# Performance work log

Measured on AMD Instinct MI355X. Metric: run time of the kernel, lower is better.

The kernel has to match this reference:

```python
import jax, jax.numpy as jnp
import numpy as np

# 8 directional offsets (dy, dx) for the -1 tap of each 3x3 filter, filter index 0..7
OFFSETS = [(-1, -1), (-1, 0), (-1, 1), (0, -1), (0, 1), (1, -1), (1, 0), (1, 1)]
# pairing used by the original prod(dim=-1): [[0,4],[1,5],[2,6],[3,7]]
PAIRS = np.array([[0, 4], [1, 5], [2, 6], [3, 7]])


def box_mean(x, k):
    """Uniform k x k box-filter mean with zero padding (same as F.conv2d with ones/k^2)."""
    kern = jnp.ones((1, 1, k, k), x.dtype) / (k * k)
    return jax.lax.conv_general_dilated(
        x, kern, window_strides=(1, 1), padding=[(k // 2, k // 2)] * 2,
        dimension_numbers=('NCHW', 'OIHW', 'NCHW'))


def pcm_scale(l, d):
    """Dilated directional diffs (center minus shifted-by-d neighbor, zero pad),
    opposite-pair products, then min over the 4 pairs."""
    b, c, h, w = l.shape
    p = jnp.pad(l, ((0, 0), (0, 0), (d, d), (d, d)))
    # shifted[..., i][y, x] = l[y + dy*d, x + dx*d] (zeros outside)
    shifted = jnp.stack(
        [p[:, :, d + dy * d:d + dy * d + h, d + dx * d:d + dx * d + w]
         for dy, dx in OFFSETS], axis=-1)  # (b,c,h,w,8)
    diff = l[..., None] - shifted          # PCM_i = conv2d(l, filter_i, dilation=d)
    temp = diff[..., PAIRS].prod(axis=-1)  # (b,c,h,w,4)
    return temp.min(axis=-1)               # (b,c,h,w)


def mpcm(x):
    outs = [pcm_scale(box_mean(x, k), k) for k in (3, 5, 7, 9)]
    return jnp.stack(outs, axis=-1).max(axis=-1)


def setup_inputs() -> dict:
    key = jax.random.key(0)
    input_tensor = jax.random.uniform(key, (16, 1, 512, 512), dtype=jnp.float32)
    return {"input_tensor": input_tensor}


def reference(input_tensor):
    out = mpcm(input_tensor)
    # per-image threshold: mean + 3 * unbiased std (torch .std default ddof=1)
    mean = out.mean(axis=(1, 2, 3), keepdims=True)
    std = out.std(axis=(1, 2, 3), keepdims=True, ddof=1)
    th = mean + 3.0 * std
    return (out > th).astype(out.dtype)
```

## Files before the change

### kernel.cpp

```cpp
#include <hip/hip_runtime.h>


namespace {

constexpr int H = 512, W = 512, NIMG = 16;
constexpr int T = 32;
constexpr int HALO = 13;
constexpr int IN = T + 2 * HALO;
constexpr int TILES = H / T;
constexpr int NT = 256;
constexpr int WI = 61;
constexpr int LSTR = 52;

struct Smem {
  double I[59 * WI];
  union alignas(16) {
    float  inf[IN * 61];
    double L[50 * LSTR];
    double red[8];
  } u;
};

template <int K>
__device__ __forceinline__ void scale_pass(Smem& s, int y0, int x0, double mp[4]) {
  constexpr int R  = K / 2;
  constexpr int LK = T + 2 * K;
  constexpr int HP = LK / 2;
  constexpr int NP = LK * HP;
  constexpr double inv = 1.0 / (double)(K * K);
  const int tid = threadIdx.x;

  for (int pe = tid; pe < NP; pe += NT) {
    const int yy = pe / HP;
    const int xx = (pe - yy * HP) * 2;
    const int iy  = yy + (HALO - K);
    const int ixm = xx + (HALO - K) - R;
    const double* Ia = s.I + (iy - R) * WI + ixm;
    const double* Ib = s.I + (iy + R + 1) * WI + ixm;
    const double a0 = Ia[0], a1 = Ia[1], aK = Ia[K], aK1 = Ia[K + 1];
    const double b0 = Ib[0], b1 = Ib[1], bK = Ib[K], bK1 = Ib[K + 1];
    const double s0 = (bK  - aK)  - (b0 - a0);
    const double s1 = (bK1 - aK1) - (b1 - a1);
    const int gy = y0 - K + yy, gx = x0 - K + xx;
    const bool in0 = ((unsigned)gy < (unsigned)H) & ((unsigned)gx < (unsigned)W);
    const bool in1 = ((unsigned)gy < (unsigned)H) & ((unsigned)(gx + 1) < (unsigned)W);
    double2 o;
    o.x = in0 ? s0 * inv : 0.0;
    o.y = in1 ? s1 * inv : 0.0;
    *(double2*)&s.u.L[yy * LSTR + xx] = o;
  }
  __syncthreads();

#pragma unroll
  for (int j = 0; j < 2; ++j) {
    const int r  = (tid >> 4) + j * 16;
    const int cc = (tid & 15) * 2;
    const double* up  = &s.u.L[r * LSTR + cc];
    const double* mid = &s.u.L[(r + K) * LSTR + cc];
    const double* dn  = &s.u.L[(r + 2 * K) * LSTR + cc];
    const double u0 = up[0],  u1 = up[1],  uK = up[K],  uK1 = up[K + 1],  u2 = up[2 * K],  u21 = up[2 * K + 1];
    const double m0 = mid[0], m1 = mid[1], mK = mid[K], mK1 = mid[K + 1], m2 = mid[2 * K], m21 = mid[2 * K + 1];
    const double w0 = dn[0],  w1 = dn[1],  wK = dn[K],  wK1 = dn[K + 1],  w2 = dn[2 * K],  w21 = dn[2 * K + 1];
    {
      const double c = mK;
      const double e0 = c - u0, e1 = c - uK, e2 = c - u2, e3 = c - m0;
      const double e4 = c - m2, e5 = c - w0, e6 = c - wK, e7 = c - w2;
      const double m = fmin(fmin(e0 * e4, e1 * e5), fmin(e2 * e6, e3 * e7));
      mp[2 * j] = fmax(mp[2 * j], m);
    }
    {
      const double c = mK1;
      const double e0 = c - u1, e1 = c - uK1, e2 = c - u21, e3 = c - m1;
      const double e4 = c - m21, e5 = c - w1, e6 = c - wK1, e7 = c - w21;
      const double m = fmin(fmin(e0 * e4, e1 * e5), fmin(e2 * e6, e3 * e7));
      mp[2 * j + 1] = fmax(mp[2 * j + 1], m);
    }
  }
  __syncthreads();
}

__device__ __forceinline__ void compute_tile(Smem& s, const float* __restrict__ img,
                                             int y0, int x0, double mp[4]) {
  const int tid = threadIdx.x;
  for (int e = tid; e < IN * IN; e += NT) {
    const int iy = e / IN, ix = e - iy * IN;
    const int gy = y0 - HALO + iy, gx = x0 - HALO + ix;
    float v = 0.0f;
    if ((unsigned)gy < (unsigned)H && (unsigned)gx < (unsigned)W) v = img[gy * W + gx];
    s.u.inf[iy * 61 + ix] = v;
  }
  for (int e = tid; e < WI; e += NT) s.I[e] = 0.0;
  for (int e = tid; e < 59; e += NT) s.I[e * WI] = 0.0;
  __syncthreads();

  if (tid < IN) {
    const float* src = &s.u.inf[tid * 61];
    double* dst = &s.I[(tid + 1) * WI + 1];
#pragma unroll
    for (int x = 0; x < IN; x += 2) {
      const float f0 = src[x], f1 = src[x + 1];
      const double r0 = (x ? dst[x - 1] : 0.0);
      const double v0 = r0 + (double)f0;
      const double v1 = v0 + (double)f1;
      dst[x] = v0; dst[x + 1] = v1;
    }
  }
  __syncthreads();

  if (tid < IN) {
    double* p = &s.I[WI + (tid + 1)];
    double run = 0.0;
#pragma unroll
    for (int y = 0; y < IN; y += 2) {
      const double v0 = p[0], v1 = p[WI];
      const double r0 = run + v0;
      run = r0 + v1;
      p[0] = r0; p[WI] = run;
      p += 2 * WI;
    }
  }
  __syncthreads();

  mp[0] = mp[1] = mp[2] = mp[3] = -1.0e300;
  scale_pass<3>(s, y0, x0, mp);
  scale_pass<5>(s, y0, x0, mp);
  scale_pass<7>(s, y0, x0, mp);
  scale_pass<9>(s, y0, x0, mp);
}

__global__ __launch_bounds__(NT, 3) void k_stats(const float* __restrict__ in,
                                                 double* __restrict__ partials,
                                                 double* __restrict__ wsmp) {
  __shared__ Smem s;
  const int img = blockIdx.z, tyb = blockIdx.y, txb = blockIdx.x;
  const int y0 = tyb * T, x0 = txb * T;
  double mp[4];
  compute_tile(s, in + (size_t)img * H * W, y0, x0, mp);

  const int tid = threadIdx.x;
  if (wsmp != nullptr) {
#pragma unroll
    for (int j = 0; j < 2; ++j) {
      const int r = (tid >> 4) + j * 16, cc = (tid & 15) * 2;
      double2 v; v.x = mp[2 * j]; v.y = mp[2 * j + 1];
      *(double2*)&wsmp[(size_t)img * H * W + (size_t)(y0 + r) * W + (x0 + cc)] = v;
    }
  }

  double s1 = (mp[0] + mp[1]) + (mp[2] + mp[3]);
  double s2 = (mp[0] * mp[0] + mp[1] * mp[1]) + (mp[2] * mp[2] + mp[3] * mp[3]);
#pragma unroll
  for (int off = 32; off; off >>= 1) {
    s1 += __shfl_down(s1, off);
    s2 += __shfl_down(s2, off);
  }
  if ((tid & 63) == 0) { s.u.red[tid >> 6] = s1; s.u.red[4 + (tid >> 6)] = s2; }
  __syncthreads();
  if (tid == 0) {
    const int bl = (img * TILES + tyb) * TILES + txb;
    partials[2 * bl]     = (s.u.red[0] + s.u.red[1]) + (s.u.red[2] + s.u.red[3]);
    partials[2 * bl + 1] = (s.u.red[4] + s.u.red[5]) + (s.u.red[6] + s.u.red[7]);
  }
}

__global__ void k_thresh(const double* __restrict__ partials, double* __restrict__ th) {
  const int img = threadIdx.x;
  if (img < NIMG) {
    double S = 0.0, S2 = 0.0;
    const int nb = TILES * TILES;
    for (int b = 0; b < nb; ++b) {
      S  += partials[2 * (img * nb + b)];
      S2 += partials[2 * (img * nb + b) + 1];
    }
    const double N = (double)(H * W);
    const double mean = S / N;
    double var = (S2 - S * S / N) / (N - 1.0);
    if (var < 0.0) var = 0.0;
    th[img] = mean + 3.0 * sqrt(var);
  }
}

__global__ __launch_bounds__(NT) void k_out_cached(const double* __restrict__ wsmp,
                                                   const double* __restrict__ th,
                                                   float* __restrict__ out) {
  const int n = NIMG * H * W / 2;
  for (int i = blockIdx.x * NT + threadIdx.x; i < n; i += gridDim.x * NT) {
    const double t = th[i >> 17];
    const double2 v = ((const double2*)wsmp)[i];
    float2 o; o.x = (v.x > t) ? 1.0f : 0.0f; o.y = (v.y > t) ? 1.0f : 0.0f;
    ((float2*)out)[i] = o;
  }
}

__global__ __launch_bounds__(NT, 3) void k_out_full(const float* __restrict__ in,
                                                    const double* __restrict__ th,
                                                    float* __restrict__ out) {
  __shared__ Smem s;
  const int img = blockIdx.z, tyb = blockIdx.y, txb = blockIdx.x;
  const int y0 = tyb * T, x0 = txb * T;
  double mp[4];
  compute_tile(s, in + (size_t)img * H * W, y0, x0, mp);
  const double t = th[img];
  const int tid = threadIdx.x;
#pragma unroll
  for (int j = 0; j < 2; ++j) {
    const int r = (tid >> 4) + j * 16, cc = (tid & 15) * 2;
    float2 o;
    o.x = (mp[2 * j]     > t) ? 1.0f : 0.0f;
    o.y = (mp[2 * j + 1] > t) ? 1.0f : 0.0f;
    *(float2*)&out[(size_t)img * H * W + (size_t)(y0 + r) * W + (x0 + cc)] = o;
  }
}

}

extern "C" void kernel_launch(void* const* d_in, const int* in_sizes, int n_in,
                              void* d_out, int out_size, void* d_ws, size_t ws_size,
                              hipStream_t stream) {
  const float* in = (const float*)d_in[0];
  float* out = (float*)d_out;

  double* th = (double*)d_ws;
  double* partials = (double*)((char*)d_ws + 4096);
  double* wsmp = (double*)((char*)d_ws + 131072);
  const bool cache = ws_size >= (size_t)131072 + (size_t)NIMG * H * W * 8;

  dim3 grid(TILES, TILES, NIMG);
  k_stats<<<grid, NT, 0, stream>>>(in, partials, cache ? wsmp : nullptr);
  k_thresh<<<1, 64, 0, stream>>>(partials, th);
  if (cache) {
    k_out_cached<<<2048, NT, 0, stream>>>(wsmp, th, out);
  } else {
    k_out_full<<<grid, NT, 0, stream>>>(in, th, out);
  }
}
```

Measured before the change: 110.8 us.

## Switch to 64x16 rectangular tiles and simplify integral-image construction

Changes the per-block tile from 32x32 to 64 wide by 16 tall, so each warp covers full 64-column rows. The input is loaded straight into the double integral-image buffer, and the row and column prefix scans become simple sequential loops instead of a separate float staging pass. The stencil stage now reads neighbors with paired double2 loads. The wider halo-to-tile ratio vertically raises redundant halo work, and the row scan covers 90 columns serially, both traded for better coalescing and fewer passes.

```diff
diff --git a/kernel.cpp b/kernel.cpp
--- a/kernel.cpp
+++ b/kernel.cpp
@@ -4,41 +4,43 @@
 namespace {
 
 constexpr int H = 512, W = 512, NIMG = 16;
-constexpr int T = 32;
+constexpr int TW = 64, TH = 16;
 constexpr int HALO = 13;
-constexpr int IN = T + 2 * HALO;
-constexpr int TILES = H / T;
+constexpr int IR = TH + 2 * HALO + 1;
+constexpr int IC = TW + 2 * HALO + 1;
+constexpr int WI = IC;
 constexpr int NT = 256;
-constexpr int WI = 61;
-constexpr int LSTR = 52;
+constexpr int LS = 82;
 
 struct Smem {
-  double I[59 * WI];
   union alignas(16) {
-    float  inf[IN * 61];
-    double L[50 * LSTR];
+    double L[34 * LS];
     double red[8];
   } u;
+  double I[IR * WI];
 };
 
 template <int K>
 __device__ __forceinline__ void scale_pass(Smem& s, int y0, int x0, double mp[4]) {
-  constexpr int R  = K / 2;
-  constexpr int LK = T + 2 * K;
-  constexpr int HP = LK / 2;
-  constexpr int NP = LK * HP;
+  constexpr int R   = K / 2;
+  constexpr int LH  = TH + 2 * K;
+  constexpr int LW  = TW + 2 * K;
+  constexpr int HPW = LW / 2;
+  constexpr int NP  = LH * HPW;
   constexpr double inv = 1.0 / (double)(K * K);
   const int tid = threadIdx.x;
 
   for (int pe = tid; pe < NP; pe += NT) {
-    const int yy = pe / HP;
-    const int xx = (pe - yy * HP) * 2;
-    const int iy  = yy + (HALO - K);
-    const int ixm = xx + (HALO - K) - R;
-    const double* Ia = s.I + (iy - R) * WI + ixm;
-    const double* Ib = s.I + (iy + R + 1) * WI + ixm;
-    const double a0 = Ia[0], a1 = Ia[1], aK = Ia[K], aK1 = Ia[K + 1];
-    const double b0 = Ib[0], b1 = Ib[1], bK = Ib[K], bK1 = Ib[K + 1];
+    const int yy = pe / HPW;
+    const int xx = (pe - yy * HPW) * 2;
+    const int li = yy + (HALO - K);
+    const int lj = xx + (HALO - K) - R;
+    const double* Ia = s.I + (li - R) * WI + lj;
+    const double* Ib = Ia + K * WI;
+    const double a0 = Ia[0], aK = Ia[K];
+    const double a1 = Ia[1], aK1 = Ia[K + 1];
+    const double b0 = Ib[0], bK = Ib[K];
+    const double b1 = Ib[1], bK1 = Ib[K + 1];
     const double s0 = (bK  - aK)  - (b0 - a0);
     const double s1 = (bK1 - aK1) - (b1 - a1);
     const int gy = y0 - K + yy, gx = x0 - K + xx;
@@ -47,31 +49,37 @@
     double2 o;
     o.x = in0 ? s0 * inv : 0.0;
     o.y = in1 ? s1 * inv : 0.0;
-    *(double2*)&s.u.L[yy * LSTR + xx] = o;
+    *(double2*)&s.u.L[yy * LS + xx] = o;
   }
   __syncthreads();
 
 #pragma unroll
   for (int j = 0; j < 2; ++j) {
-    const int r  = (tid >> 4) + j * 16;
-    const int cc = (tid & 15) * 2;
-    const double* up  = &s.u.L[r * LSTR + cc];
-    const double* mid = &s.u.L[(r + K) * LSTR + cc];
-    const double* dn  = &s.u.L[(r + 2 * K) * LSTR + cc];
-    const double u0 = up[0],  u1 = up[1],  uK = up[K],  uK1 = up[K + 1],  u2 = up[2 * K],  u21 = up[2 * K + 1];
-    const double m0 = mid[0], m1 = mid[1], mK = mid[K], mK1 = mid[K + 1], m2 = mid[2 * K], m21 = mid[2 * K + 1];
-    const double w0 = dn[0],  w1 = dn[1],  wK = dn[K],  wK1 = dn[K + 1],  w2 = dn[2 * K],  w21 = dn[2 * K + 1];
+    const int r  = (tid >> 5) + 8 * j;
+    const int cc = (tid & 31) * 2;
+    const double* up  = &s.u.L[r * LS + cc];
+    const double* mid = up + K * LS;
+    const double* dn  = up + 2 * K * LS;
+    const double2 u0p = *(const double2*)up;
+    const double  uK = up[K], uK1 = up[K + 1];
+    const double2 u2p = *(const double2*)(up + 2 * K);
+    const double2 m0p = *(const double2*)mid;
+    const double  mK = mid[K], mK1 = mid[K + 1];
+    const double2 m2p = *(const double2*)(mid + 2 * K);
+    const double2 w0p = *(const double2*)dn;
+    const double  wK = dn[K], wK1 = dn[K + 1];
+    const double2 w2p = *(const double2*)(dn + 2 * K);
     {
       const double c = mK;
-      const double e0 = c - u0, e1 = c - uK, e2 = c - u2, e3 = c - m0;
-      const double e4 = c - m2, e5 = c - w0, e6 = c - wK, e7 = c - w2;
+      const double e0 = c - u0p.x, e1 = c - uK, e2 = c - u2p.x, e3 = c - m0p.x;
+      const double e4 = c - m2p.x, e5 = c - w0p.x, e6 = c - wK, e7 = c - w2p.x;
       const double m = fmin(fmin(e0 * e4, e1 * e5), fmin(e2 * e6, e3 * e7));
       mp[2 * j] = fmax(mp[2 * j], m);
     }
     {
       const double c = mK1;
-      const double e0 = c - u1, e1 = c - uK1, e2 = c - u21, e3 = c - m1;
-      const double e4 = c - m21, e5 = c - w1, e6 = c - wK1, e7 = c - w21;
+      const double e0 = c - u0p.y, e1 = c - uK1, e2 = c - u2p.y, e3 = c - m0p.y;
+      const double e4 = c - m2p.y, e5 = c - w0p.y, e6 = c - wK1, e7 = c - w2p.y;
       const double m = fmin(fmin(e0 * e4, e1 * e5), fmin(e2 * e6, e3 * e7));
       mp[2 * j + 1] = fmax(mp[2 * j + 1], m);
     }
@@ -82,42 +90,29 @@
 __device__ __forceinline__ void compute_tile(Smem& s, const float* __restrict__ img,
                                              int y0, int x0, double mp[4]) {
   const int tid = threadIdx.x;
-  for (int e = tid; e < IN * IN; e += NT) {
-    const int iy = e / IN, ix = e - iy * IN;
-    const int gy = y0 - HALO + iy, gx = x0 - HALO + ix;
-    float v = 0.0f;
-    if ((unsigned)gy < (unsigned)H && (unsigned)gx < (unsigned)W) v = img[gy * W + gx];
-    s.u.inf[iy * 61 + ix] = v;
-  }
-  for (int e = tid; e < WI; e += NT) s.I[e] = 0.0;
-  for (int e = tid; e < 59; e += NT) s.I[e * WI] = 0.0;
-  __syncthreads();
-
-  if (tid < IN) {
-    const float* src = &s.u.inf[tid * 61];
-    double* dst = &s.I[(tid + 1) * WI + 1];
-#pragma unroll
-    for (int x = 0; x < IN; x += 2) {
-      const float f0 = src[x], f1 = src[x + 1];
-      const double r0 = (x ? dst[x - 1] : 0.0);
-      const double v0 = r0 + (double)f0;
-      const double v1 = v0 + (double)f1;
-      dst[x] = v0; dst[x + 1] = v1;
-    }
-  }
-  __syncthreads();
-
-  if (tid < IN) {
+  for (int e = tid; e < IR * IC; e += NT) {
+    const int iy = e / IC, ix = e - iy * IC;
+    const int gy = y0 - HALO + iy - 1, gx = x0 - HALO + ix - 1;
+    double v = 0.0;
+    if (iy > 0 && ix > 0 && (unsigned)gy < (unsigned)H && (unsigned)gx < (unsigned)W)
+      v = (double)img[gy * W + gx];
+    s.I[iy * WI + ix] = v;
+  }
+  __syncthreads();
+
+  if (tid < IR - 1) {
+    double* p = &s.I[(tid + 1) * WI + 1];
+    double run = 0.0;
+#pragma unroll
+    for (int x = 0; x < IC - 1; ++x) { run += p[x]; p[x] = run; }
+  }
+  __syncthreads();
+
+  if (tid < IC - 1) {
     double* p = &s.I[WI + (tid + 1)];
     double run = 0.0;
 #pragma unroll
-    for (int y = 0; y < IN; y += 2) {
-      const double v0 = p[0], v1 = p[WI];
-      const double r0 = run + v0;
-      run = r0 + v1;
-      p[0] = r0; p[WI] = run;
-      p += 2 * WI;
-    }
+    for (int y = 0; y < IR - 1; ++y) { run += *p; *p = run; p += WI; }
   }
   __syncthreads();
 
@@ -132,8 +127,8 @@
                                                  double* __restrict__ partials,
                                                  double* __restrict__ wsmp) {
   __shared__ Smem s;
-  const int img = blockIdx.z, tyb = blockIdx.y, txb = blockIdx.x;
-  const int y0 = tyb * T, x0 = txb * T;
+  const int img = blockIdx.z;
+  const int y0 = blockIdx.y * TH, x0 = blockIdx.x * TW;
   double mp[4];
   compute_tile(s, in + (size_t)img * H * W, y0, x0, mp);
 
@@ -141,7 +136,7 @@
   if (wsmp != nullptr) {
 #pragma unroll
     for (int j = 0; j < 2; ++j) {
-      const int r = (tid >> 4) + j * 16, cc = (tid & 15) * 2;
+      const int r = (tid >> 5) + 8 * j, cc = (tid & 31) * 2;
       double2 v; v.x = mp[2 * j]; v.y = mp[2 * j + 1];
       *(double2*)&wsmp[(size_t)img * H * W + (size_t)(y0 + r) * W + (x0 + cc)] = v;
     }
@@ -157,7 +152,7 @@
   if ((tid & 63) == 0) { s.u.red[tid >> 6] = s1; s.u.red[4 + (tid >> 6)] = s2; }
   __syncthreads();
   if (tid == 0) {
-    const int bl = (img * TILES + tyb) * TILES + txb;
+    const int bl = (img * gridDim.y + blockIdx.y) * gridDim.x + blockIdx.x;
     partials[2 * bl]     = (s.u.red[0] + s.u.red[1]) + (s.u.red[2] + s.u.red[3]);
     partials[2 * bl + 1] = (s.u.red[4] + s.u.red[5]) + (s.u.red[6] + s.u.red[7]);
   }
@@ -167,7 +162,7 @@
   const int img = threadIdx.x;
   if (img < NIMG) {
     double S = 0.0, S2 = 0.0;
-    const int nb = TILES * TILES;
+    const int nb = (H / TH) * (W / TW);
     for (int b = 0; b < nb; ++b) {
       S  += partials[2 * (img * nb + b)];
       S2 += partials[2 * (img * nb + b) + 1];
@@ -196,15 +191,15 @@
                                                     const double* __restrict__ th,
                                                     float* __restrict__ out) {
   __shared__ Smem s;
-  const int img = blockIdx.z, tyb = blockIdx.y, txb = blockIdx.x;
-  const int y0 = tyb * T, x0 = txb * T;
+  const int img = blockIdx.z;
+  const int y0 = blockIdx.y * TH, x0 = blockIdx.x * TW;
   double mp[4];
   compute_tile(s, in + (size_t)img * H * W, y0, x0, mp);
   const double t = th[img];
   const int tid = threadIdx.x;
 #pragma unroll
   for (int j = 0; j < 2; ++j) {
-    const int r = (tid >> 4) + j * 16, cc = (tid & 15) * 2;
+    const int r = (tid >> 5) + 8 * j, cc = (tid & 31) * 2;
     float2 o;
     o.x = (mp[2 * j]     > t) ? 1.0f : 0.0f;
     o.y = (mp[2 * j + 1] > t) ? 1.0f : 0.0f;
@@ -225,7 +220,7 @@
   double* wsmp = (double*)((char*)d_ws + 131072);
   const bool cache = ws_size >= (size_t)131072 + (size_t)NIMG * H * W * 8;
 
-  dim3 grid(TILES, TILES, NIMG);
+  dim3 grid(W / TW, H / TH, NIMG);
   k_stats<<<grid, NT, 0, stream>>>(in, partials, cache ? wsmp : nullptr);
   k_thresh<<<1, 64, 0, stream>>>(partials, th);
   if (cache) {
```

After: 117.7 us. 6.2% more time.
